# Kernel optimization log

Hardware: AMD Instinct MI355X
Metric: run time of the kernel (lower is better)

Reference implementation:

```python
import jax, jax.numpy as jnp
import numpy as np

DIM = 1024
NUM_EXPERTS = 8
TOP_K = 2
LOAD_BALANCE_WEIGHT = 0.01


def setup_inputs() -> dict:
    key = jax.random.key(0)
    ks = jax.random.split(key, 8)
    d, e, h = DIM, NUM_EXPERTS, 4 * DIM
    scale = 0.02
    return {
        "x": jax.random.normal(ks[0], (4, 2048, d), dtype=jnp.float32),
        "w_router": jax.random.normal(ks[1], (d, e), dtype=jnp.float32) * scale,
        "b_router": jnp.zeros((e,), dtype=jnp.float32),
        "w1": jax.random.normal(ks[2], (e, d, h), dtype=jnp.float32) * scale,
        "b1": jnp.zeros((e, h), dtype=jnp.float32),
        "w2": jax.random.normal(ks[3], (e, h, d), dtype=jnp.float32) * scale,
        "b2": jnp.zeros((e, d), dtype=jnp.float32),
    }


def reference(x, w_router, b_router, w1, b1, w2, b2):
    # x: [b, s, d]
    router_logits = jnp.einsum("bsd,de->bse", x, w_router) + b_router  # [b,s,E]
    probs = jax.nn.softmax(router_logits, axis=-1)
    routing_weights, selected_experts = jax.lax.top_k(probs, TOP_K)  # [b,s,K]
    routing_weights = routing_weights / routing_weights.sum(axis=-1, keepdims=True)

    output = jnp.zeros_like(x)
    for e in range(NUM_EXPERTS):
        # Dense per-expert MLP; tokens not routed to expert e get gate 0,
        # matching the masked scatter-add in the original module.
        h = jax.nn.gelu(jnp.einsum("bsd,dh->bsh", x, w1[e]) + b1[e], approximate=False)
        y = jnp.einsum("bsh,hd->bsd", h, w2[e]) + b2[e]
        gate = jnp.where(selected_experts == e, routing_weights, 0.0).sum(axis=-1)  # [b,s]
        output = output + y * gate[..., None]

    # Load-balance aux loss: var (unbiased, ddof=1) / mean of tokens-per-expert.
    one_hot = jax.nn.one_hot(selected_experts, NUM_EXPERTS, dtype=jnp.float32)  # [b,s,K,E]
    tokens_per_expert = one_hot.sum(axis=(0, 1, 2))  # [E]
    load_balance_loss = (jnp.var(tokens_per_expert, ddof=1) / tokens_per_expert.mean()) * LOAD_BALANCE_WEIGHT
    return output, load_balance_loss
```

## Files before the change

kernel.cpp:

```cpp
#include <hip/hip_runtime.h>
#include <math.h>

#define TOKENS 8192
#define DIM    1024
#define NEXP   8
#define HID    4096
#define TILE_M 128
#define MAX_TILES 136
#define BKS    32

#define BK     32
#define LDA    40
#define LDB    40

typedef __bf16 bf16x8 __attribute__((ext_vector_type(8)));
typedef float  f32x4  __attribute__((ext_vector_type(4)));
typedef unsigned int u32x4 __attribute__((ext_vector_type(4)));

__device__ __forceinline__ unsigned short f2bf(float f) {
  union { float f; unsigned u; } v; v.f = f;
  unsigned u = v.u + 0x7fffu + ((v.u >> 16) & 1u);
  return (unsigned short)(u >> 16);
}
__device__ __forceinline__ float gelu_f(float v) {
  return 0.5f * v * (1.f + erff(v * 0.7071067811865476f));
}
__device__ __forceinline__ float gelu_fast(float v) {
  float t = v * v;
  float y = 0.7978845608f * v * fmaf(t, 0.044715f, 1.0f);
  y = fminf(y, 15.f);
  float z = __expf(2.f * y);
  return v * z * __builtin_amdgcn_rcpf(1.f + z);
}
__device__ __forceinline__ void gload16(const void* g, void* l) {
  __builtin_amdgcn_global_load_lds(
      (const __attribute__((address_space(1))) void*)g,
      (__attribute__((address_space(3))) void*)l, 16, 0, 0);
}
__device__ __forceinline__ int xcd_swz(int id, int nwg) {
  int q = nwg >> 3, r = nwg & 7;
  int xcd = id & 7, rank = id >> 3;
  return (xcd < r) ? xcd * (q + 1) + rank : r * (q + 1) + (xcd - r) * q + rank;
}

__global__ __launch_bounds__(256) void k_router(
    const float* __restrict__ x, const float* __restrict__ wr,
    const float* __restrict__ br, int* __restrict__ sel,
    float* __restrict__ gates, int* __restrict__ counts,
    unsigned short* __restrict__ xb)
{
  int t = blockIdx.x * 4 + (threadIdx.x >> 6);
  int lane = threadIdx.x & 63;
  const float* xr = x + (size_t)t * DIM;
  unsigned short* xo = xb + (size_t)t * DIM;
  float acc[NEXP];
#pragma unroll
  for (int e = 0; e < NEXP; ++e) acc[e] = 0.f;
#pragma unroll
  for (int it = 0; it < 4; ++it) {
    int d = it * 256 + lane * 4;
    float4 xv = *(const float4*)(xr + d);
    ushort4 pk;
    pk.x = f2bf(xv.x); pk.y = f2bf(xv.y); pk.z = f2bf(xv.z); pk.w = f2bf(xv.w);
    *(ushort4*)(xo + d) = pk;
    float xs[4] = {xv.x, xv.y, xv.z, xv.w};
#pragma unroll
    for (int j = 0; j < 4; ++j) {
      float4 wa = *(const float4*)(wr + (size_t)(d + j) * NEXP);
      float4 wb = *(const float4*)(wr + (size_t)(d + j) * NEXP + 4);
      acc[0] += xs[j] * wa.x; acc[1] += xs[j] * wa.y;
      acc[2] += xs[j] * wa.z; acc[3] += xs[j] * wa.w;
      acc[4] += xs[j] * wb.x; acc[5] += xs[j] * wb.y;
      acc[6] += xs[j] * wb.z; acc[7] += xs[j] * wb.w;
    }
  }
#pragma unroll
  for (int off = 32; off >= 1; off >>= 1) {
#pragma unroll
    for (int e = 0; e < NEXP; ++e) acc[e] += __shfl_xor(acc[e], off);
  }
  if (lane == 0) {
    float l[NEXP];
#pragma unroll
    for (int e = 0; e < NEXP; ++e) l[e] = acc[e] + br[e];
    int e1 = 0; float v1 = l[0];
#pragma unroll
    for (int e = 1; e < NEXP; ++e) if (l[e] > v1) { v1 = l[e]; e1 = e; }
    int e2 = -1; float v2 = -1e30f;
#pragma unroll
    for (int e = 0; e < NEXP; ++e) {
      if (e == e1) continue;
      if (l[e] > v2) { v2 = l[e]; e2 = e; }
    }
    float g1 = 1.f / (1.f + expf(v2 - v1));
    sel[t * 2] = e1; sel[t * 2 + 1] = e2;
    gates[t * 2] = g1; gates[t * 2 + 1] = 1.f - g1;
    atomicAdd(&counts[e1], 1);
    atomicAdd(&counts[e2], 1);
  }
}

__global__ __launch_bounds__(256) void k_setup(
    const int* __restrict__ counts, int* __restrict__ cursors,
    int* __restrict__ ntiles_p, int* __restrict__ tile_expert,
    int* __restrict__ tile_row0, int* __restrict__ pair_token,
    float* __restrict__ pair_gate, float* __restrict__ loss_out)
{
  __shared__ int s_pad0[NEXP], s_pad1[NEXP];
  int tid = threadIdx.x;
  if (tid == 0) {
    int poff = 0, nt = 0;
    float var = 0.f;
    for (int e = 0; e < NEXP; ++e) {
      int c = counts[e];
      cursors[e] = poff;
      int ntl = (c + TILE_M - 1) / TILE_M;
      for (int i = 0; i < ntl; ++i) { tile_expert[nt] = e; tile_row0[nt] = poff + i * TILE_M; ++nt; }
      s_pad0[e] = poff + c;
      s_pad1[e] = poff + ntl * TILE_M;
      float d = (float)c - 2048.f;
      var += d * d;
      poff += ntl * TILE_M;
    }
    *ntiles_p = nt;
    *loss_out = (var * (1.f / 7.f)) * (1.f / 2048.f) * 0.01f;
  }
  __syncthreads();
#pragma unroll
  for (int e = 0; e < NEXP; ++e) {
    for (int r = s_pad0[e] + tid; r < s_pad1[e]; r += 256) {
      pair_token[r] = -1; pair_gate[r] = 0.f;
    }
  }
}

__global__ __launch_bounds__(256) void k_bucket(
    const int* __restrict__ sel, const float* __restrict__ gates,
    int* __restrict__ cursors, int* __restrict__ pair_token, float* __restrict__ pair_gate)
{
  int t = blockIdx.x * 256 + threadIdx.x;
#pragma unroll
  for (int k = 0; k < 2; ++k) {
    int e = sel[t * 2 + k];
    int pos = atomicAdd(&cursors[e], 1);
    pair_token[pos] = t;
    pair_gate[pos] = gates[t * 2 + k];
  }
}

__global__ __launch_bounds__(256) void k_castwT(
    const float* __restrict__ w, unsigned short* __restrict__ wT, int K, int N)
{
  __shared__ unsigned short t[64][72];
  int e = blockIdx.z, n0 = blockIdx.x * 64, k0 = blockIdx.y * 64;
  int tid = threadIdx.x;
  int kr = tid >> 2, nc = (tid & 3) * 16;
  const float* src = w + ((size_t)e * K + k0 + kr) * N + n0 + nc;
#pragma unroll
  for (int j = 0; j < 4; ++j) {
    f32x4 v = *(const f32x4*)(src + j * 4);
#pragma unroll
    for (int q = 0; q < 4; ++q) t[nc + j * 4 + q][kr] = f2bf(v[q]);
  }
  __syncthreads();
  int nr = tid >> 2, kc = (tid & 3) * 16;
  unsigned short* dst = wT + ((size_t)e * N + n0 + nr) * K + k0 + kc;
  *(u32x4*)dst = *(const u32x4*)&t[nr][kc];
  *(u32x4*)(dst + 8) = *(const u32x4*)&t[nr][kc + 8];
}

__global__ __launch_bounds__(256) void k_gemm1n(
    const unsigned short* __restrict__ xb, const unsigned short* __restrict__ w1T,
    const float* __restrict__ b1, const int* __restrict__ pair_token,
    const int* __restrict__ tile_expert, const int* __restrict__ tile_row0,
    const int* __restrict__ ntiles_p, unsigned short* __restrict__ h, int chunk_base)
{
  const int NBn = HID / 128;
  const int nwg = gridDim.x;
  int newid = xcd_swz(blockIdx.x, nwg);
  int ltile = newid / NBn, nb = newid - ltile * NBn;
  int tile = chunk_base + ltile;
  if (tile >= *ntiles_p) return;
  const int e = tile_expert[tile];
  const int row0 = tile_row0[tile];
  const int n0 = nb * 128;
  const int tid = threadIdx.x;
  const int w = tid >> 6, lane = tid & 63;

  __shared__ unsigned short As[3][128 * BKS];
  __shared__ unsigned short Bs[3][128 * BKS];
  __shared__ int tok[128];

  if (tid < 128) { int t = pair_token[row0 + tid]; tok[tid] = (t < 0) ? 0 : t; }
  __syncthreads();

  const int sr = lane >> 2;
  const int kq = (lane & 3) * 8;
  const int ar1 = w * 32 + sr, ar2 = ar1 + 16;
  const unsigned short* ag1 = xb + (size_t)tok[ar1] * DIM + kq;
  const unsigned short* ag2 = xb + (size_t)tok[ar2] * DIM + kq;
  const unsigned short* bg1 = w1T + ((size_t)e * HID + n0 + ar1) * DIM + kq;
  const unsigned short* bg2 = w1T + ((size_t)e * HID + n0 + ar2) * DIM + kq;

  const int wm = (w & 1) * 64, wn = (w >> 1) * 64;
  const int lr = lane & 15, lk = lane >> 4;

  f32x4 acc[4][4];
#pragma unroll
  for (int mi = 0; mi < 4; ++mi)
#pragma unroll
    for (int ni = 0; ni < 4; ++ni) acc[mi][ni] = {0.f, 0.f, 0.f, 0.f};

#define STAGE1(buf, koff)                                      \
  gload16(ag1 + (koff), &As[buf][(w * 32) * BKS]);             \
  gload16(ag2 + (koff), &As[buf][(w * 32 + 16) * BKS]);        \
  gload16(bg1 + (koff), &Bs[buf][(w * 32) * BKS]);             \
  gload16(bg2 + (koff), &Bs[buf][(w * 32 + 16) * BKS]);

  STAGE1(0, 0)
  STAGE1(1, BKS)
  asm volatile("s_waitcnt vmcnt(4)" ::: "memory");
  __builtin_amdgcn_s_barrier();

  const int NT = DIM / BKS;
  int cur = 0, dst = 2;
  for (int t = 0; t < NT; ++t) {
    if (t + 2 < NT) { STAGE1(dst, (t + 2) * BKS) }
    bf16x8 af[4], bfr[4];
#pragma unroll
    for (int mi = 0; mi < 4; ++mi)
      af[mi] = *(const bf16x8*)&As[cur][(wm + mi * 16 + lr) * BKS + lk * 8];
#pragma unroll
    for (int ni = 0; ni < 4; ++ni)
      bfr[ni] = *(const bf16x8*)&Bs[cur][(wn + ni * 16 + lr) * BKS + lk * 8];
    asm volatile("s_waitcnt lgkmcnt(0)" ::: "memory");
    __builtin_amdgcn_sched_barrier(0);
    __builtin_amdgcn_s_setprio(1);
#pragma unroll
    for (int mi = 0; mi < 4; ++mi)
#pragma unroll
      for (int ni = 0; ni < 4; ++ni)
        acc[mi][ni] = __builtin_amdgcn_mfma_f32_16x16x32_bf16(bfr[ni], af[mi], acc[mi][ni], 0, 0, 0);
    __builtin_amdgcn_s_setprio(0);
    if (t + 2 < NT) { asm volatile("s_waitcnt vmcnt(4)" ::: "memory"); }
    else            { asm volatile("s_waitcnt vmcnt(0)" ::: "memory"); }
    __builtin_amdgcn_s_barrier();
    cur = (cur == 2) ? 0 : cur + 1;
    dst = (dst == 2) ? 0 : dst + 1;
  }
#undef STAGE1

  const size_t tl = (size_t)(tile - chunk_base);
  f32x4 bv[4];
#pragma unroll
  for (int ni = 0; ni < 4; ++ni)
    bv[ni] = *(const f32x4*)(b1 + (size_t)e * HID + n0 + wn + ni * 16 + lk * 4);
#pragma unroll
  for (int mi = 0; mi < 4; ++mi) {
    int m = wm + mi * 16 + lr;
    unsigned short* hrow = h + (tl * TILE_M + m) * HID + n0;
#pragma unroll
    for (int ni = 0; ni < 4; ++ni) {
      int nb4 = wn + ni * 16 + lk * 4;
      ushort4 pk;
      pk.x = f2bf(gelu_fast(acc[mi][ni][0] + bv[ni][0]));
      pk.y = f2bf(gelu_fast(acc[mi][ni][1] + bv[ni][1]));
      pk.z = f2bf(gelu_fast(acc[mi][ni][2] + bv[ni][2]));
      pk.w = f2bf(gelu_fast(acc[mi][ni][3] + bv[ni][3]));
      *(ushort4*)(hrow + nb4) = pk;
    }
  }
}

__global__ __launch_bounds__(256) void k_gemm2n(
    const unsigned short* __restrict__ h, const unsigned short* __restrict__ w2T,
    const float* __restrict__ b2, const int* __restrict__ pair_token,
    const float* __restrict__ pair_gate,
    const int* __restrict__ tile_expert, const int* __restrict__ tile_row0,
    const int* __restrict__ ntiles_p, float* __restrict__ out, int chunk_base)
{
  const int NBn = DIM / 128;
  const int nwg = gridDim.x;
  int newid = xcd_swz(blockIdx.x, nwg);
  int ltile = newid / NBn, nb = newid - ltile * NBn;
  int tile = chunk_base + ltile;
  if (tile >= *ntiles_p) return;
  const int e = tile_expert[tile];
  const int row0 = tile_row0[tile];
  const int n0 = nb * 128;
  const int tid = threadIdx.x;
  const int w = tid >> 6, lane = tid & 63;

  __shared__ unsigned short As[3][128 * BKS];
  __shared__ unsigned short Bs[3][128 * BKS];
  __shared__ int tok[128];
  __shared__ float gat[128];

  if (tid < 128) { tok[tid] = pair_token[row0 + tid]; gat[tid] = pair_gate[row0 + tid]; }
  __syncthreads();

  const int sr = lane >> 2;
  const int kq = (lane & 3) * 8;
  const int ar1 = w * 32 + sr, ar2 = ar1 + 16;
  const size_t tl = (size_t)(tile - chunk_base);
  const unsigned short* ag1 = h + (tl * TILE_M + ar1) * HID + kq;
  const unsigned short* ag2 = h + (tl * TILE_M + ar2) * HID + kq;
  const unsigned short* bg1 = w2T + ((size_t)e * DIM + n0 + ar1) * HID + kq;
  const unsigned short* bg2 = w2T + ((size_t)e * DIM + n0 + ar2) * HID + kq;

  const int wm = (w & 1) * 64, wn = (w >> 1) * 64;
  const int lr = lane & 15, lk = lane >> 4;

  f32x4 acc[4][4];
#pragma unroll
  for (int mi = 0; mi < 4; ++mi)
#pragma unroll
    for (int ni = 0; ni < 4; ++ni) acc[mi][ni] = {0.f, 0.f, 0.f, 0.f};

#define STAGE2(buf, koff)                                      \
  gload16(ag1 + (koff), &As[buf][(w * 32) * BKS]);             \
  gload16(ag2 + (koff), &As[buf][(w * 32 + 16) * BKS]);        \
  gload16(bg1 + (koff), &Bs[buf][(w * 32) * BKS]);             \
  gload16(bg2 + (koff), &Bs[buf][(w * 32 + 16) * BKS]);

  STAGE2(0, 0)
  STAGE2(1, BKS)
  asm volatile("s_waitcnt vmcnt(4)" ::: "memory");
  __builtin_amdgcn_s_barrier();

  const int NT = HID / BKS;
  int cur = 0, dst = 2;
  for (int t = 0; t < NT; ++t) {
    if (t + 2 < NT) { STAGE2(dst, (t + 2) * BKS) }
    bf16x8 af[4], bfr[4];
#pragma unroll
    for (int mi = 0; mi < 4; ++mi)
      af[mi] = *(const bf16x8*)&As[cur][(wm + mi * 16 + lr) * BKS + lk * 8];
#pragma unroll
    for (int ni = 0; ni < 4; ++ni)
      bfr[ni] = *(const bf16x8*)&Bs[cur][(wn + ni * 16 + lr) * BKS + lk * 8];
    asm volatile("s_waitcnt lgkmcnt(0)" ::: "memory");
    __builtin_amdgcn_sched_barrier(0);
    __builtin_amdgcn_s_setprio(1);
#pragma unroll
    for (int mi = 0; mi < 4; ++mi)
#pragma unroll
      for (int ni = 0; ni < 4; ++ni)
        acc[mi][ni] = __builtin_amdgcn_mfma_f32_16x16x32_bf16(af[mi], bfr[ni], acc[mi][ni], 0, 0, 0);
    __builtin_amdgcn_s_setprio(0);
    if (t + 2 < NT) { asm volatile("s_waitcnt vmcnt(4)" ::: "memory"); }
    else            { asm volatile("s_waitcnt vmcnt(0)" ::: "memory"); }
    __builtin_amdgcn_s_barrier();
    cur = (cur == 2) ? 0 : cur + 1;
    dst = (dst == 2) ? 0 : dst + 1;
  }
#undef STAGE2

  float bia[4];
#pragma unroll
  for (int ni = 0; ni < 4; ++ni) bia[ni] = b2[(size_t)e * DIM + n0 + wn + ni * 16 + lr];
#pragma unroll
  for (int mi = 0; mi < 4; ++mi)
#pragma unroll
    for (int r = 0; r < 4; ++r) {
      int m = wm + mi * 16 + lk * 4 + r;
      int t = tok[m];
      if (t >= 0) {
        float g = gat[m];
#pragma unroll
        for (int ni = 0; ni < 4; ++ni) {
          int n = wn + ni * 16 + lr;
          atomicAdd(out + (size_t)t * DIM + n0 + n, (acc[mi][ni][r] + bia[ni]) * g);
        }
      }
    }
}

__global__ __launch_bounds__(256) void k_gemm1(
    const unsigned short* __restrict__ xb, const float* __restrict__ w1,
    const float* __restrict__ b1, const int* __restrict__ pair_token,
    const int* __restrict__ tile_expert, const int* __restrict__ tile_row0,
    const int* __restrict__ ntiles_p, unsigned short* __restrict__ h, int chunk_base)
{
  int tile = chunk_base + blockIdx.y;
  if (tile >= *ntiles_p) return;
  const int e = tile_expert[tile];
  const int row0 = tile_row0[tile];
  const int n0 = blockIdx.x * 128;
  const int tid = threadIdx.x;

  __shared__ unsigned short As[TILE_M * LDA];
  __shared__ unsigned short Bs[128 * LDB];
  __shared__ int tok[TILE_M];

  if (tid < TILE_M) tok[tid] = pair_token[row0 + tid];
  __syncthreads();

  const int ar = tid >> 1, akh = (tid & 1) * 16;
  const int bk = tid >> 3, bnh = (tid & 7) * 16;
  const int bswz = tid & 3;
  const int wv = tid >> 6, lane = tid & 63;
  const int wm = (wv & 1) * 64, wn = (wv >> 1) * 64;
  const int lr = lane & 15, lk = lane >> 4;
  const int atok = tok[ar];

  f32x4 acc[4][4];
#pragma unroll
  for (int mi = 0; mi < 4; ++mi)
#pragma unroll
    for (int ni = 0; ni < 4; ++ni) acc[mi][ni] = {0.f, 0.f, 0.f, 0.f};

  const unsigned short* asrc = (atok >= 0) ? (xb + (size_t)atok * DIM + akh) : (const unsigned short*)0;
  const float* bsrc0 = w1 + ((size_t)e * DIM + bk) * HID + n0 + bnh;
  const int wcol = 8 * ((bk >> 3) ^ bswz) + (bk & 7);

  for (int k0 = 0; k0 < DIM; k0 += BK) {
    u32x4 av0 = {0, 0, 0, 0}, av1 = {0, 0, 0, 0};
    if (asrc) {
      av0 = *(const u32x4*)(asrc + k0);
      av1 = *(const u32x4*)(asrc + k0 + 8);
    }
    float bv[16];
    const float* bs = bsrc0 + (size_t)k0 * HID;
#pragma unroll
    for (int j = 0; j < 4; ++j) {
      f32x4 f = *(const f32x4*)(bs + j * 4);
      bv[j * 4 + 0] = f[0]; bv[j * 4 + 1] = f[1];
      bv[j * 4 + 2] = f[2]; bv[j * 4 + 3] = f[3];
    }
    __syncthreads();
    *(u32x4*)&As[ar * LDA + akh] = av0;
    *(u32x4*)&As[ar * LDA + akh + 8] = av1;
#pragma unroll
    for (int j = 0; j < 16; ++j)
      Bs[(bnh + j) * LDB + wcol] = f2bf(bv[j]);
    __syncthreads();

    bf16x8 af[4], bfr[4];
#pragma unroll
    for (int mi = 0; mi < 4; ++mi)
      af[mi] = *(const bf16x8*)&As[(wm + mi * 16 + lr) * LDA + lk * 8];
#pragma unroll
    for (int ni = 0; ni < 4; ++ni) {
      int pch = lk ^ (((wn >> 4) + ni) & 3);
      bfr[ni] = *(const bf16x8*)&Bs[(wn + ni * 16 + lr) * LDB + pch * 8];
    }
#pragma unroll
    for (int mi = 0; mi < 4; ++mi)
#pragma unroll
      for (int ni = 0; ni < 4; ++ni)
        acc[mi][ni] = __builtin_amdgcn_mfma_f32_16x16x32_bf16(af[mi], bfr[ni], acc[mi][ni], 0, 0, 0);
  }

  const size_t tl = (size_t)(tile - chunk_base);
#pragma unroll
  for (int mi = 0; mi < 4; ++mi)
#pragma unroll
    for (int ni = 0; ni < 4; ++ni)
#pragma unroll
      for (int r = 0; r < 4; ++r) {
        int m = wm + mi * 16 + (lane >> 4) * 4 + r;
        int n = wn + ni * 16 + (lane & 15);
        float v = acc[mi][ni][r] + b1[(size_t)e * HID + n0 + n];
        h[(tl * TILE_M + m) * HID + n0 + n] = f2bf(gelu_f(v));
      }
}

__global__ __launch_bounds__(256) void k_gemm2(
    const unsigned short* __restrict__ h, const float* __restrict__ w2,
    const float* __restrict__ b2, const int* __restrict__ pair_token,
    const float* __restrict__ pair_gate,
    const int* __restrict__ tile_expert, const int* __restrict__ tile_row0,
    const int* __restrict__ ntiles_p, float* __restrict__ out, int chunk_base)
{
  int tile = chunk_base + blockIdx.y;
  if (tile >= *ntiles_p) return;
  const int e = tile_expert[tile];
  const int row0 = tile_row0[tile];
  const int n0 = blockIdx.x * 128;
  const int tid = threadIdx.x;

  __shared__ unsigned short As[TILE_M * LDA];
  __shared__ unsigned short Bs[128 * LDB];
  __shared__ int tok[TILE_M];
  __shared__ float gat[TILE_M];

  if (tid < TILE_M) { tok[tid] = pair_token[row0 + tid]; gat[tid] = pair_gate[row0 + tid]; }
  __syncthreads();

  const int ar = tid >> 1, akh = (tid & 1) * 16;
  const int bk = tid >> 3, bnh = (tid & 7) * 16;
  const int bswz = tid & 3;
  const int wv = tid >> 6, lane = tid & 63;
  const int wm = (wv & 1) * 64, wn = (wv >> 1) * 64;
  const int lr = lane & 15, lk = lane >> 4;

  f32x4 acc[4][4];
#pragma unroll
  for (int mi = 0; mi < 4; ++mi)
#pragma unroll
    for (int ni = 0; ni < 4; ++ni) acc[mi][ni] = {0.f, 0.f, 0.f, 0.f};

  const size_t tl = (size_t)(tile - chunk_base);
  const unsigned short* asrc = h + (tl * TILE_M + ar) * HID + akh;
  const float* bsrc0 = w2 + ((size_t)e * HID + bk) * DIM + n0 + bnh;
  const int wcol = 8 * ((bk >> 3) ^ bswz) + (bk & 7);

  for (int k0 = 0; k0 < HID; k0 += BK) {
    u32x4 av0 = *(const u32x4*)(asrc + k0);
    u32x4 av1 = *(const u32x4*)(asrc + k0 + 8);
    float bv[16];
    const float* bs = bsrc0 + (size_t)k0 * DIM;
#pragma unroll
    for (int j = 0; j < 4; ++j) {
      f32x4 f = *(const f32x4*)(bs + j * 4);
      bv[j * 4 + 0] = f[0]; bv[j * 4 + 1] = f[1];
      bv[j * 4 + 2] = f[2]; bv[j * 4 + 3] = f[3];
    }
    __syncthreads();
    *(u32x4*)&As[ar * LDA + akh] = av0;
    *(u32x4*)&As[ar * LDA + akh + 8] = av1;
#pragma unroll
    for (int j = 0; j < 16; ++j)
      Bs[(bnh + j) * LDB + wcol] = f2bf(bv[j]);
    __syncthreads();

    bf16x8 af[4], bfr[4];
#pragma unroll
    for (int mi = 0; mi < 4; ++mi)
      af[mi] = *(const bf16x8*)&As[(wm + mi * 16 + lr) * LDA + lk * 8];
#pragma unroll
    for (int ni = 0; ni < 4; ++ni) {
      int pch = lk ^ (((wn >> 4) + ni) & 3);
      bfr[ni] = *(const bf16x8*)&Bs[(wn + ni * 16 + lr) * LDB + pch * 8];
    }
#pragma unroll
    for (int mi = 0; mi < 4; ++mi)
#pragma unroll
      for (int ni = 0; ni < 4; ++ni)
        acc[mi][ni] = __builtin_amdgcn_mfma_f32_16x16x32_bf16(af[mi], bfr[ni], acc[mi][ni], 0, 0, 0);
  }

#pragma unroll
  for (int mi = 0; mi < 4; ++mi)
#pragma unroll
    for (int ni = 0; ni < 4; ++ni)
#pragma unroll
      for (int r = 0; r < 4; ++r) {
        int m = wm + mi * 16 + (lane >> 4) * 4 + r;
        int n = wn + ni * 16 + (lane & 15);
        int t = tok[m];
        if (t >= 0) {
          float v = acc[mi][ni][r] + b2[(size_t)e * DIM + n0 + n];
          atomicAdd(out + (size_t)t * DIM + n0 + n, v * gat[m]);
        }
      }
}

extern "C" void kernel_launch(void* const* d_in, const int* in_sizes, int n_in,
                              void* d_out, int out_size, void* d_ws, size_t ws_size,
                              hipStream_t stream) {
  const float* x  = (const float*)d_in[0];
  const float* wr = (const float*)d_in[1];
  const float* br = (const float*)d_in[2];
  const float* w1 = (const float*)d_in[3];
  const float* b1 = (const float*)d_in[4];
  const float* w2 = (const float*)d_in[5];
  const float* b2 = (const float*)d_in[6];
  float* out = (float*)d_out;

  char* ws = (char*)d_ws;
  int*   counts      = (int*)(ws + 0);
  int*   cursors     = (int*)(ws + 64);
  int*   ntiles      = (int*)(ws + 128);
  int*   tile_expert = (int*)(ws + 256);
  int*   tile_row0   = (int*)(ws + 1024);
  int*   sel         = (int*)(ws + 4096);
  float* gates       = (float*)(ws + 4096 + 65536);
  int*   pair_token  = (int*)(ws + 4096 + 131072);
  float* pair_gate   = (float*)(ws + 4096 + 131072 + 69632);

  const size_t OFF_XB  = 274432;
  const size_t XB_SZ   = (size_t)TOKENS * DIM * 2;
  const size_t OFF_W1T = OFF_XB + XB_SZ;
  const size_t WT_SZ   = (size_t)NEXP * DIM * HID * 2;
  const size_t OFF_W2T = OFF_W1T + WT_SZ;
  const size_t OFF_HN  = OFF_W2T + WT_SZ;
  const size_t tile_bytes = (size_t)TILE_M * HID * 2;

  unsigned short* xb  = (unsigned short*)(ws + OFF_XB);

  hipMemsetAsync(d_out, 0, (size_t)out_size * sizeof(float), stream);
  hipMemsetAsync(counts, 0, 64, stream);

  hipLaunchKernelGGL(k_router, dim3(TOKENS / 4), dim3(256), 0, stream,
                     x, wr, br, sel, gates, counts, xb);
  hipLaunchKernelGGL(k_setup, dim3(1), dim3(256), 0, stream,
                     counts, cursors, ntiles, tile_expert, tile_row0,
                     pair_token, pair_gate, out + (size_t)out_size - 1);
  hipLaunchKernelGGL(k_bucket, dim3(TOKENS / 256), dim3(256), 0, stream,
                     sel, gates, cursors, pair_token, pair_gate);

  bool newpath = ws_size >= OFF_HN + tile_bytes;

  if (newpath) {
    unsigned short* w1T = (unsigned short*)(ws + OFF_W1T);
    unsigned short* w2T = (unsigned short*)(ws + OFF_W2T);
    unsigned short* h   = (unsigned short*)(ws + OFF_HN);

    hipLaunchKernelGGL(k_castwT, dim3(HID / 64, DIM / 64, NEXP), dim3(256), 0, stream,
                       w1, w1T, DIM, HID);
    hipLaunchKernelGGL(k_castwT, dim3(DIM / 64, HID / 64, NEXP), dim3(256), 0, stream,
                       w2, w2T, HID, DIM);

    long long avail = (long long)ws_size - (long long)OFF_HN;
    int tpc = (int)(avail / (long long)tile_bytes);
    if (tpc < 1) tpc = 1;
    if (tpc > MAX_TILES) tpc = MAX_TILES;
    int nchunks = (MAX_TILES + tpc - 1) / tpc;

    for (int c = 0; c < nchunks; ++c) {
      hipLaunchKernelGGL(k_gemm1n, dim3(tpc * (HID / 128)), dim3(256), 0, stream,
                         xb, w1T, b1, pair_token, tile_expert, tile_row0, ntiles, h, c * tpc);
      hipLaunchKernelGGL(k_gemm2n, dim3(tpc * (DIM / 128)), dim3(256), 0, stream,
                         h, w2T, b2, pair_token, pair_gate, tile_expert, tile_row0, ntiles, out, c * tpc);
    }
  } else {
    unsigned short* h = (unsigned short*)(ws + OFF_W1T);
    long long avail = (long long)ws_size - (long long)OFF_W1T;
    int tpc = (avail > 0) ? (int)(avail / (long long)tile_bytes) : 0;
    if (tpc < 1) tpc = 1;
    if (tpc > MAX_TILES) tpc = MAX_TILES;
    int nchunks = (MAX_TILES + tpc - 1) / tpc;

    for (int c = 0; c < nchunks; ++c) {
      hipLaunchKernelGGL(k_gemm1, dim3(HID / 128, tpc), dim3(256), 0, stream,
                         xb, w1, b1, pair_token, tile_expert, tile_row0, ntiles, h, c * tpc);
      hipLaunchKernelGGL(k_gemm2, dim3(DIM / 128, tpc), dim3(256), 0, stream,
                         h, w2, b2, pair_token, pair_gate, tile_expert, tile_row0, ntiles, out, c * tpc);
    }
  }
}
```

Before: 827.8 us.

## Enlarge grouped MoE GEMM tiles to 128x256 with 8 waves, BK=64, swizzled LDS

Both expert GEMM kernels now use 512-thread blocks computing 128x256 output tiles, with the K step doubled to 64 and an XOR-swizzled LDS layout to avoid bank conflicts. The goal is more reuse of each staged A tile across N, fewer barriers per FLOP, and less LDS conflict stall. In exchange, LDS use grows to about 144KB per block, which limits occupancy and leaves fewer workgroups per tile chunk. The LDS and wave layout must also line up with the unchanged epilogue indexing.

After: 963.2 us. 1.16x slower.

```diff
diff --git a/kernel.cpp b/kernel.cpp
--- a/kernel.cpp
+++ b/kernel.cpp
@@ -7,7 +7,6 @@
 #define HID    4096
 #define TILE_M 128
 #define MAX_TILES 136
-#define BKS    32
 
 #define BK     32
 #define LDA    40
@@ -169,41 +168,43 @@
   *(u32x4*)(dst + 8) = *(const u32x4*)&t[nr][kc + 8];
 }
 
-__global__ __launch_bounds__(256) void k_gemm1n(
+__global__ __launch_bounds__(512) void k_gemm1n(
     const unsigned short* __restrict__ xb, const unsigned short* __restrict__ w1T,
     const float* __restrict__ b1, const int* __restrict__ pair_token,
     const int* __restrict__ tile_expert, const int* __restrict__ tile_row0,
     const int* __restrict__ ntiles_p, unsigned short* __restrict__ h, int chunk_base)
 {
-  const int NBn = HID / 128;
-  const int nwg = gridDim.x;
-  int newid = xcd_swz(blockIdx.x, nwg);
+  const int NBn = HID / 256;
+  int newid = xcd_swz(blockIdx.x, gridDim.x);
   int ltile = newid / NBn, nb = newid - ltile * NBn;
   int tile = chunk_base + ltile;
   if (tile >= *ntiles_p) return;
   const int e = tile_expert[tile];
   const int row0 = tile_row0[tile];
-  const int n0 = nb * 128;
+  const int n0 = nb * 256;
   const int tid = threadIdx.x;
   const int w = tid >> 6, lane = tid & 63;
 
-  __shared__ unsigned short As[3][128 * BKS];
-  __shared__ unsigned short Bs[3][128 * BKS];
+  __shared__ unsigned short As[3][128 * 64];
+  __shared__ unsigned short Bs[3][256 * 64];
   __shared__ int tok[128];
 
   if (tid < 128) { int t = pair_token[row0 + tid]; tok[tid] = (t < 0) ? 0 : t; }
   __syncthreads();
 
-  const int sr = lane >> 2;
-  const int kq = (lane & 3) * 8;
-  const int ar1 = w * 32 + sr, ar2 = ar1 + 16;
-  const unsigned short* ag1 = xb + (size_t)tok[ar1] * DIM + kq;
-  const unsigned short* ag2 = xb + (size_t)tok[ar2] * DIM + kq;
-  const unsigned short* bg1 = w1T + ((size_t)e * HID + n0 + ar1) * DIM + kq;
-  const unsigned short* bg2 = w1T + ((size_t)e * HID + n0 + ar2) * DIM + kq;
+  const int rg  = lane >> 3;
+  const int swz = ((lane & 7) ^ rg) * 8;
+  const unsigned short* ag0 = xb + (size_t)tok[w * 16 + rg] * DIM + swz;
+  const unsigned short* ag1 = xb + (size_t)tok[w * 16 + 8 + rg] * DIM + swz;
+  const size_t bbase = (size_t)e * HID + n0 + w * 32;
+  const unsigned short* bg0 = w1T + (bbase + rg) * DIM + swz;
+  const unsigned short* bg1 = w1T + (bbase + 8 + rg) * DIM + swz;
+  const unsigned short* bg2 = w1T + (bbase + 16 + rg) * DIM + swz;
+  const unsigned short* bg3 = w1T + (bbase + 24 + rg) * DIM + swz;
 
   const int wm = (w & 1) * 64, wn = (w >> 1) * 64;
   const int lr = lane & 15, lk = lane >> 4;
+  const int rs = (lr & 7);
 
   f32x4 acc[4][4];
 #pragma unroll
@@ -211,28 +212,34 @@
 #pragma unroll
     for (int ni = 0; ni < 4; ++ni) acc[mi][ni] = {0.f, 0.f, 0.f, 0.f};
 
-#define STAGE1(buf, koff)                                      \
-  gload16(ag1 + (koff), &As[buf][(w * 32) * BKS]);             \
-  gload16(ag2 + (koff), &As[buf][(w * 32 + 16) * BKS]);        \
-  gload16(bg1 + (koff), &Bs[buf][(w * 32) * BKS]);             \
-  gload16(bg2 + (koff), &Bs[buf][(w * 32 + 16) * BKS]);
+#define STAGE1(buf, koff)                                  \
+  gload16(ag0 + (koff), &As[buf][(w * 16) * 64]);          \
+  gload16(ag1 + (koff), &As[buf][(w * 16 + 8) * 64]);      \
+  gload16(bg0 + (koff), &Bs[buf][(w * 32) * 64]);          \
+  gload16(bg1 + (koff), &Bs[buf][(w * 32 + 8) * 64]);      \
+  gload16(bg2 + (koff), &Bs[buf][(w * 32 + 16) * 64]);     \
+  gload16(bg3 + (koff), &Bs[buf][(w * 32 + 24) * 64]);
 
   STAGE1(0, 0)
-  STAGE1(1, BKS)
-  asm volatile("s_waitcnt vmcnt(4)" ::: "memory");
+  STAGE1(1, 64)
+  asm volatile("s_waitcnt vmcnt(6)" ::: "memory");
   __builtin_amdgcn_s_barrier();
 
-  const int NT = DIM / BKS;
+  const int NT = DIM / 64;
   int cur = 0, dst = 2;
   for (int t = 0; t < NT; ++t) {
-    if (t + 2 < NT) { STAGE1(dst, (t + 2) * BKS) }
-    bf16x8 af[4], bfr[4];
-#pragma unroll
-    for (int mi = 0; mi < 4; ++mi)
-      af[mi] = *(const bf16x8*)&As[cur][(wm + mi * 16 + lr) * BKS + lk * 8];
+    if (t + 2 < NT) { STAGE1(dst, (t + 2) * 64) }
+    bf16x8 af[4][2], bfr[4][2];
+#pragma unroll
+    for (int mi = 0; mi < 4; ++mi)
+#pragma unroll
+      for (int ks = 0; ks < 2; ++ks)
+        af[mi][ks] = *(const bf16x8*)&As[cur][(wm + mi * 16 + lr) * 64 + ((ks * 4 + lk) ^ rs) * 8];
 #pragma unroll
     for (int ni = 0; ni < 4; ++ni)
-      bfr[ni] = *(const bf16x8*)&Bs[cur][(wn + ni * 16 + lr) * BKS + lk * 8];
+#pragma unroll
+      for (int ks = 0; ks < 2; ++ks)
+        bfr[ni][ks] = *(const bf16x8*)&Bs[cur][(wn + ni * 16 + lr) * 64 + ((ks * 4 + lk) ^ rs) * 8];
     asm volatile("s_waitcnt lgkmcnt(0)" ::: "memory");
     __builtin_amdgcn_sched_barrier(0);
     __builtin_amdgcn_s_setprio(1);
@@ -240,9 +247,11 @@
     for (int mi = 0; mi < 4; ++mi)
 #pragma unroll
       for (int ni = 0; ni < 4; ++ni)
-        acc[mi][ni] = __builtin_amdgcn_mfma_f32_16x16x32_bf16(bfr[ni], af[mi], acc[mi][ni], 0, 0, 0);
+#pragma unroll
+        for (int ks = 0; ks < 2; ++ks)
+          acc[mi][ni] = __builtin_amdgcn_mfma_f32_16x16x32_bf16(bfr[ni][ks], af[mi][ks], acc[mi][ni], 0, 0, 0);
     __builtin_amdgcn_s_setprio(0);
-    if (t + 2 < NT) { asm volatile("s_waitcnt vmcnt(4)" ::: "memory"); }
+    if (t + 2 < NT) { asm volatile("s_waitcnt vmcnt(6)" ::: "memory"); }
     else            { asm volatile("s_waitcnt vmcnt(0)" ::: "memory"); }
     __builtin_amdgcn_s_barrier();
     cur = (cur == 2) ? 0 : cur + 1;
@@ -272,44 +281,46 @@
   }
 }
 
-__global__ __launch_bounds__(256) void k_gemm2n(
+__global__ __launch_bounds__(512) void k_gemm2n(
     const unsigned short* __restrict__ h, const unsigned short* __restrict__ w2T,
     const float* __restrict__ b2, const int* __restrict__ pair_token,
     const float* __restrict__ pair_gate,
     const int* __restrict__ tile_expert, const int* __restrict__ tile_row0,
     const int* __restrict__ ntiles_p, float* __restrict__ out, int chunk_base)
 {
-  const int NBn = DIM / 128;
-  const int nwg = gridDim.x;
-  int newid = xcd_swz(blockIdx.x, nwg);
+  const int NBn = DIM / 256;
+  int newid = xcd_swz(blockIdx.x, gridDim.x);
   int ltile = newid / NBn, nb = newid - ltile * NBn;
   int tile = chunk_base + ltile;
   if (tile >= *ntiles_p) return;
   const int e = tile_expert[tile];
   const int row0 = tile_row0[tile];
-  const int n0 = nb * 128;
+  const int n0 = nb * 256;
   const int tid = threadIdx.x;
   const int w = tid >> 6, lane = tid & 63;
 
-  __shared__ unsigned short As[3][128 * BKS];
-  __shared__ unsigned short Bs[3][128 * BKS];
+  __shared__ unsigned short As[3][128 * 64];
+  __shared__ unsigned short Bs[3][256 * 64];
   __shared__ int tok[128];
   __shared__ float gat[128];
 
   if (tid < 128) { tok[tid] = pair_token[row0 + tid]; gat[tid] = pair_gate[row0 + tid]; }
   __syncthreads();
 
-  const int sr = lane >> 2;
-  const int kq = (lane & 3) * 8;
-  const int ar1 = w * 32 + sr, ar2 = ar1 + 16;
+  const int rg  = lane >> 3;
+  const int swz = ((lane & 7) ^ rg) * 8;
   const size_t tl = (size_t)(tile - chunk_base);
-  const unsigned short* ag1 = h + (tl * TILE_M + ar1) * HID + kq;
-  const unsigned short* ag2 = h + (tl * TILE_M + ar2) * HID + kq;
-  const unsigned short* bg1 = w2T + ((size_t)e * DIM + n0 + ar1) * HID + kq;
-  const unsigned short* bg2 = w2T + ((size_t)e * DIM + n0 + ar2) * HID + kq;
+  const unsigned short* ag0 = h + (tl * TILE_M + w * 16 + rg) * HID + swz;
+  const unsigned short* ag1 = h + (tl * TILE_M + w * 16 + 8 + rg) * HID + swz;
+  const size_t bbase = (size_t)e * DIM + n0 + w * 32;
+  const unsigned short* bg0 = w2T + (bbase + rg) * HID + swz;
+  const unsigned short* bg1 = w2T + (bbase + 8 + rg) * HID + swz;
+  const unsigned short* bg2 = w2T + (bbase + 16 + rg) * HID + swz;
+  const unsigned short* bg3 = w2T + (bbase + 24 + rg) * HID + swz;
 
   const int wm = (w & 1) * 64, wn = (w >> 1) * 64;
   const int lr = lane & 15, lk = lane >> 4;
+  const int rs = (lr & 7);
 
   f32x4 acc[4][4];
 #pragma unroll
@@ -317,28 +328,34 @@
 #pragma unroll
     for (int ni = 0; ni < 4; ++ni) acc[mi][ni] = {0.f, 0.f, 0.f, 0.f};
 
-#define STAGE2(buf, koff)                                      \
-  gload16(ag1 + (koff), &As[buf][(w * 32) * BKS]);             \
-  gload16(ag2 + (koff), &As[buf][(w * 32 + 16) * BKS]);        \
-  gload16(bg1 + (koff), &Bs[buf][(w * 32) * BKS]);             \
-  gload16(bg2 + (koff), &Bs[buf][(w * 32 + 16) * BKS]);
+#define STAGE2(buf, koff)                                  \
+  gload16(ag0 + (koff), &As[buf][(w * 16) * 64]);          \
+  gload16(ag1 + (koff), &As[buf][(w * 16 + 8) * 64]);      \
+  gload16(bg0 + (koff), &Bs[buf][(w * 32) * 64]);          \
+  gload16(bg1 + (koff), &Bs[buf][(w * 32 + 8) * 64]);      \
+  gload16(bg2 + (koff), &Bs[buf][(w * 32 + 16) * 64]);     \
+  gload16(bg3 + (koff), &Bs[buf][(w * 32 + 24) * 64]);
 
   STAGE2(0, 0)
-  STAGE2(1, BKS)
-  asm volatile("s_waitcnt vmcnt(4)" ::: "memory");
+  STAGE2(1, 64)
+  asm volatile("s_waitcnt vmcnt(6)" ::: "memory");
   __builtin_amdgcn_s_barrier();
 
-  const int NT = HID / BKS;
+  const int NT = HID / 64;
   int cur = 0, dst = 2;
   for (int t = 0; t < NT; ++t) {
-    if (t + 2 < NT) { STAGE2(dst, (t + 2) * BKS) }
-    bf16x8 af[4], bfr[4];
-#pragma unroll
-    for (int mi = 0; mi < 4; ++mi)
-      af[mi] = *(const bf16x8*)&As[cur][(wm + mi * 16 + lr) * BKS + lk * 8];
+    if (t + 2 < NT) { STAGE2(dst, (t + 2) * 64) }
+    bf16x8 af[4][2], bfr[4][2];
+#pragma unroll
+    for (int mi = 0; mi < 4; ++mi)
+#pragma unroll
+      for (int ks = 0; ks < 2; ++ks)
+        af[mi][ks] = *(const bf16x8*)&As[cur][(wm + mi * 16 + lr) * 64 + ((ks * 4 + lk) ^ rs) * 8];
 #pragma unroll
     for (int ni = 0; ni < 4; ++ni)
-      bfr[ni] = *(const bf16x8*)&Bs[cur][(wn + ni * 16 + lr) * BKS + lk * 8];
+#pragma unroll
+      for (int ks = 0; ks < 2; ++ks)
+        bfr[ni][ks] = *(const bf16x8*)&Bs[cur][(wn + ni * 16 + lr) * 64 + ((ks * 4 + lk) ^ rs) * 8];
     asm volatile("s_waitcnt lgkmcnt(0)" ::: "memory");
     __builtin_amdgcn_sched_barrier(0);
     __builtin_amdgcn_s_setprio(1);
@@ -346,9 +363,11 @@
     for (int mi = 0; mi < 4; ++mi)
 #pragma unroll
       for (int ni = 0; ni < 4; ++ni)
-        acc[mi][ni] = __builtin_amdgcn_mfma_f32_16x16x32_bf16(af[mi], bfr[ni], acc[mi][ni], 0, 0, 0);
+#pragma unroll
+        for (int ks = 0; ks < 2; ++ks)
+          acc[mi][ni] = __builtin_amdgcn_mfma_f32_16x16x32_bf16(af[mi][ks], bfr[ni][ks], acc[mi][ni], 0, 0, 0);
     __builtin_amdgcn_s_setprio(0);
-    if (t + 2 < NT) { asm volatile("s_waitcnt vmcnt(4)" ::: "memory"); }
+    if (t + 2 < NT) { asm volatile("s_waitcnt vmcnt(6)" ::: "memory"); }
     else            { asm volatile("s_waitcnt vmcnt(0)" ::: "memory"); }
     __builtin_amdgcn_s_barrier();
     cur = (cur == 2) ? 0 : cur + 1;
@@ -620,9 +639,9 @@
     int nchunks = (MAX_TILES + tpc - 1) / tpc;
 
     for (int c = 0; c < nchunks; ++c) {
-      hipLaunchKernelGGL(k_gemm1n, dim3(tpc * (HID / 128)), dim3(256), 0, stream,
+      hipLaunchKernelGGL(k_gemm1n, dim3(tpc * (HID / 256)), dim3(512), 0, stream,
                          xb, w1T, b1, pair_token, tile_expert, tile_row0, ntiles, h, c * tpc);
-      hipLaunchKernelGGL(k_gemm2n, dim3(tpc * (DIM / 128)), dim3(256), 0, stream,
+      hipLaunchKernelGGL(k_gemm2n, dim3(tpc * (DIM / 256)), dim3(512), 0, stream,
                          h, w2T, b2, pair_token, pair_gate, tile_expert, tile_row0, ntiles, out, c * tpc);
     }
   } else {
```
